# Kernel tuning notes

Hardware: AMD Instinct MI355X
Metric: run time of the kernel (lower is better)

The kernel has to match this reference:

```python
import jax, jax.numpy as jnp
import numpy as np

DIM = 512; H = 8; DH = 64; M = 256; ITERS = 6; K = 33  # residual conv kernel


def _pinv(x, iters=ITERS):
    # Moore-Penrose iterative pseudo-inverse (lucidrains moore_penrose_iter_pinv)
    abs_x = jnp.abs(x)
    denom = abs_x.sum(-1).max() * abs_x.sum(-2).max()  # global max of col/row sums
    z = jnp.swapaxes(x, -1, -2) / denom
    I = jnp.eye(x.shape[-1], dtype=x.dtype)
    for _ in range(iters):
        xz = x @ z
        z = 0.25 * z @ (13. * I - xz @ (15. * I - xz @ (7. * I - xz)))
    return z


def setup_inputs() -> dict:
    key = jax.random.key(0)
    ks = jax.random.split(key, 5)
    b, n = 4, 4096
    inner = H * DH
    x = jax.random.normal(ks[0], (b, n, DIM), jnp.float32)
    ln_g = jnp.ones((DIM,), jnp.float32)
    ln_b = jnp.zeros((DIM,), jnp.float32)
    w_qkv = jax.random.normal(ks[1], (DIM, 3 * inner), jnp.float32) / np.sqrt(DIM).astype(np.float32)
    w_out = jax.random.normal(ks[2], (inner, DIM), jnp.float32) / np.sqrt(inner).astype(np.float32)
    b_out = jnp.zeros((DIM,), jnp.float32)
    res_w = jax.random.normal(ks[3], (H, K), jnp.float32) * 0.02  # depthwise conv weight per head
    return {"x": x, "ln_g": ln_g, "ln_b": ln_b, "w_qkv": w_qkv,
            "w_out": w_out, "b_out": b_out, "res_w": res_w}


def reference(x, ln_g, ln_b, w_qkv, w_out, b_out, res_w):
    b, n, d = x.shape
    # LayerNorm (eps=1e-5, biased variance, like torch)
    mu = x.mean(-1, keepdims=True)
    var = ((x - mu) ** 2).mean(-1, keepdims=True)
    xn = (x - mu) * jax.lax.rsqrt(var + 1e-5) * ln_g + ln_b
    # QKV projection, no bias
    qkv = xn @ w_qkv  # [b, n, 3*h*dh]
    q, k, v = jnp.split(qkv, 3, axis=-1)
    tohd = lambda t: t.reshape(b, n, H, DH).transpose(0, 2, 1, 3)  # b h n d
    q = tohd(q) * (DH ** -0.5)
    k = tohd(k)
    v = tohd(v)
    # landmarks: mean over consecutive blocks of l = n // M (n divisible by M here)
    l = n // M
    q_l = q.reshape(b, H, M, l, DH).mean(3)  # b h m d
    k_l = k.reshape(b, H, M, l, DH).mean(3)
    attn1 = jax.nn.softmax(jnp.einsum('bhid,bhjd->bhij', q, k_l), axis=-1)   # b h n m
    attn2 = jax.nn.softmax(jnp.einsum('bhid,bhjd->bhij', q_l, k_l), axis=-1)  # b h m m
    attn3 = jax.nn.softmax(jnp.einsum('bhid,bhjd->bhij', q_l, k), axis=-1)   # b h m n
    out = (attn1 @ _pinv(attn2)) @ (attn3 @ v)  # b h n dh
    # depthwise residual conv over sequence dim (Conv2d(heads, heads, (33,1), groups=heads))
    res = jax.lax.conv_general_dilated(
        v, res_w.reshape(H, 1, K, 1), (1, 1), ((K // 2, K // 2), (0, 0)),
        feature_group_count=H, dimension_numbers=('NCHW', 'OIHW', 'NCHW'))
    out = out + res
    # merge heads + output projection (dropout is identity at eval)
    out = out.transpose(0, 2, 1, 3).reshape(b, n, H * DH) @ w_out + b_out
    # TransLayer residual
    return x + out
```

## Files before the change

### kernel.cpp

```cpp
#include <hip/hip_runtime.h>
#include <hip/hip_bf16.h>

#define SEQ    4096
#define NBAT   4
#define NHEAD  8
#define NBH    32
#define DMODEL 512
#define DHEAD  64
#define NLM    256

typedef __attribute__((ext_vector_type(8))) short s8v;
typedef __attribute__((ext_vector_type(4))) float f4v;

__device__ __forceinline__ float b2f(unsigned short u){
  union { unsigned int i; float f; } v; v.i = ((unsigned int)u) << 16; return v.f;
}
__device__ __forceinline__ unsigned short f2b(float f){
  union { float f; unsigned int i; } v; v.f = f;
  unsigned int r = v.i + 0x7fffu + ((v.i >> 16) & 1u);
  return (unsigned short)(r >> 16);
}
__device__ __forceinline__ s8v ldg8(const unsigned short* p){
  return *reinterpret_cast<const s8v*>(p);
}
__device__ __forceinline__ f4v mfma16(s8v a, s8v b, f4v c){
  return __builtin_amdgcn_mfma_f32_16x16x32_bf16(a, b, c, 0, 0, 0);
}
__device__ __forceinline__ f4v zero4(){ f4v z; z[0]=0.f; z[1]=0.f; z[2]=0.f; z[3]=0.f; return z; }

__global__ void k_prep(const float* __restrict__ wqkv, const float* __restrict__ wout,
                       unsigned short* __restrict__ wqkvT, unsigned short* __restrict__ woutT,
                       unsigned int* __restrict__ denomU, float* __restrict__ w2f){
  int t = blockIdx.x*256 + threadIdx.x;
  if (t == 0) denomU[0] = 0u;
  if (t < 786432){ int kk = t/1536, n = t%1536; wqkvT[(size_t)n*512 + kk] = f2b(wqkv[t]); }
  else { int t2 = t - 786432; if (t2 < 262144){ int kk = t2/512, n = t2%512; woutT[(size_t)n*512 + kk] = f2b(wout[t2]); } }
  if (t < 524288) w2f[t] = 0.f;
}

__global__ __launch_bounds__(256) void k_ln(const float* __restrict__ x, const float* __restrict__ g,
                                            const float* __restrict__ be, unsigned short* __restrict__ xn){
  int row = blockIdx.x*4 + (threadIdx.x>>6);
  int l = threadIdx.x & 63;
  const float* xr = x + (size_t)row*DMODEL;
  float4 a = *(const float4*)(xr + l*4);
  float4 b = *(const float4*)(xr + 256 + l*4);
  float s = a.x+a.y+a.z+a.w + b.x+b.y+b.z+b.w;
  float q = a.x*a.x+a.y*a.y+a.z*a.z+a.w*a.w + b.x*b.x+b.y*b.y+b.z*b.z+b.w*b.w;
  #pragma unroll
  for (int m=1;m<64;m<<=1){ s += __shfl_xor(s,m); q += __shfl_xor(q,m); }
  float mean = s*(1.f/DMODEL);
  float rstd = rsqrtf(q*(1.f/DMODEL) - mean*mean + 1e-5f);
  int c0 = l*4, c1 = 256 + l*4;
  float av[4] = {a.x,a.y,a.z,a.w}, bv[4] = {b.x,b.y,b.z,b.w};
  ushort4 u0, u1;
  unsigned short* p0 = (unsigned short*)&u0; unsigned short* p1 = (unsigned short*)&u1;
  #pragma unroll
  for (int e=0;e<4;++e){
    p0[e] = f2b((av[e]-mean)*rstd*g[c0+e] + be[c0+e]);
    p1[e] = f2b((bv[e]-mean)*rstd*g[c1+e] + be[c1+e]);
  }
  *(ushort4*)(xn + (size_t)row*DMODEL + c0) = u0;
  *(ushort4*)(xn + (size_t)row*DMODEL + c1) = u1;
}

__device__ __forceinline__ void gemm512(const unsigned short* __restrict__ A, const unsigned short* __restrict__ B,
                                        int m0, int n0, int t, unsigned short* lA, unsigned short* lB,
                                        f4v acc[4][4]){
  int w = t>>6, l = t&63;
  int wm = (w&1)*64, wn = (w>>1)*64;
  for (int ks=0; ks<16; ++ks){
    #pragma unroll
    for (int it=0; it<2; ++it){
      int cid = it*256 + t; int r = cid>>2, kof = (cid&3)<<3;
      *(s8v*)&lA[r*40 + kof] = ldg8(&A[(size_t)(m0+r)*DMODEL + ks*32 + kof]);
      *(s8v*)&lB[r*40 + kof] = ldg8(&B[(size_t)(n0+r)*DMODEL + ks*32 + kof]);
    }
    __syncthreads();
    s8v af[4], bf[4];
    #pragma unroll
    for (int i=0;i<4;++i) af[i] = *(s8v*)&lA[(wm+i*16+(l&15))*40 + ((l>>4)<<3)];
    #pragma unroll
    for (int j=0;j<4;++j) bf[j] = *(s8v*)&lB[(wn+j*16+(l&15))*40 + ((l>>4)<<3)];
    #pragma unroll
    for (int i=0;i<4;++i)
      #pragma unroll
      for (int j=0;j<4;++j) acc[i][j] = mfma16(af[i], bf[j], acc[i][j]);
    __syncthreads();
  }
}

__global__ __launch_bounds__(256) void k_gqkv(const unsigned short* __restrict__ xn, const unsigned short* __restrict__ wT,
                                              unsigned short* __restrict__ q, unsigned short* __restrict__ k,
                                              unsigned short* __restrict__ v, unsigned short* __restrict__ vT){
  __shared__ unsigned short lA[128*40], lB[128*40];
  int bid = blockIdx.x; int mblk = bid/12, nblk = bid%12;
  int m0 = mblk*128, n0 = nblk*128;
  int t = threadIdx.x;
  f4v acc[4][4];
  #pragma unroll
  for (int i=0;i<4;++i)
    #pragma unroll
    for (int j=0;j<4;++j) acc[i][j] = zero4();
  gemm512(xn, wT, m0, n0, t, lA, lB, acc);
  int w = t>>6, l = t&63; int wm = (w&1)*64, wn = (w>>1)*64;
  int part = nblk >> 2;
  int coff = (nblk & 3) * 128;
  unsigned short* dst = (part==0) ? q : (part==1) ? k : v;
  float scale = (part==0) ? 0.125f : 1.f;
  #pragma unroll
  for (int i=0;i<4;++i)
  #pragma unroll
  for (int j=0;j<4;++j){
    int colg = coff + wn + j*16 + (l&15);
    int h = colg>>6, c = colg&63;
    #pragma unroll
    for (int r=0;r<4;++r){
      int rowg = m0 + wm + i*16 + ((l>>4)<<2) + r;
      int b = rowg>>12, n = rowg&4095;
      unsigned short val = f2b(acc[i][j][r]*scale);
      dst[ (((size_t)(b*NHEAD + h))*SEQ + n)*DHEAD + c ] = val;
      if (part == 2)
        vT[ (((size_t)(b*NHEAD + h))*DHEAD + c)*SEQ + n ] = val;
    }
  }
}

__global__ __launch_bounds__(256) void k_gout(const unsigned short* __restrict__ ao, const unsigned short* __restrict__ wT,
                                              const float* __restrict__ x, const float* __restrict__ bo,
                                              float* __restrict__ out){
  __shared__ unsigned short lA[128*40], lB[128*40];
  int bid = blockIdx.x; int mblk = bid>>2, nblk = bid&3;
  int m0 = mblk*128, n0 = nblk*128;
  int t = threadIdx.x;
  f4v acc[4][4];
  #pragma unroll
  for (int i=0;i<4;++i)
    #pragma unroll
    for (int j=0;j<4;++j) acc[i][j] = zero4();
  gemm512(ao, wT, m0, n0, t, lA, lB, acc);
  int w = t>>6, l = t&63; int wm = (w&1)*64, wn = (w>>1)*64;
  #pragma unroll
  for (int i=0;i<4;++i)
  #pragma unroll
  for (int j=0;j<4;++j){
    int colg = n0 + wn + j*16 + (l&15);
    #pragma unroll
    for (int r=0;r<4;++r){
      int rowg = m0 + wm + i*16 + ((l>>4)<<2) + r;
      size_t ad = (size_t)rowg*DMODEL + colg;
      out[ad] = acc[i][j][r] + x[ad] + bo[colg];
    }
  }
}

__global__ void k_lmk(const unsigned short* __restrict__ q, const unsigned short* __restrict__ k,
                      unsigned short* __restrict__ ql, unsigned short* __restrict__ kl){
  int tg = blockIdx.x*256 + threadIdx.x;
  int c4 = (tg&15)*4, m = (tg>>4)&255, bh = tg>>12;
  const unsigned short* qb = q + ((size_t)bh*SEQ + m*16)*DHEAD + c4;
  const unsigned short* kb = k + ((size_t)bh*SEQ + m*16)*DHEAD + c4;
  float s0=0.f,s1=0.f,s2=0.f,s3=0.f, t0=0.f,t1=0.f,t2=0.f,t3=0.f;
  #pragma unroll
  for (int j=0;j<16;++j){
    ushort4 uq = *(const ushort4*)(qb + (size_t)j*DHEAD);
    ushort4 uk = *(const ushort4*)(kb + (size_t)j*DHEAD);
    s0+=b2f(uq.x); s1+=b2f(uq.y); s2+=b2f(uq.z); s3+=b2f(uq.w);
    t0+=b2f(uk.x); t1+=b2f(uk.y); t2+=b2f(uk.z); t3+=b2f(uk.w);
  }
  ushort4 oq, ok;
  oq.x=f2b(s0*(1.f/16.f)); oq.y=f2b(s1*(1.f/16.f)); oq.z=f2b(s2*(1.f/16.f)); oq.w=f2b(s3*(1.f/16.f));
  ok.x=f2b(t0*(1.f/16.f)); ok.y=f2b(t1*(1.f/16.f)); ok.z=f2b(t2*(1.f/16.f)); ok.w=f2b(t3*(1.f/16.f));
  *(ushort4*)(ql + ((size_t)bh*NLM + m)*DHEAD + c4) = oq;
  *(ushort4*)(kl + ((size_t)bh*NLM + m)*DHEAD + c4) = ok;
}

__global__ __launch_bounds__(512) void k_attn2(const unsigned short* __restrict__ ql, const unsigned short* __restrict__ kl,
                                               unsigned short* __restrict__ a2, unsigned short* __restrict__ a2t,
                                               unsigned int* __restrict__ denomU){
  __shared__ float cs[256];
  int bh = blockIdx.x; int t = threadIdx.x; int w = t>>6, l = t&63;
  const unsigned short* Q = ql + (size_t)bh*NLM*DHEAD;
  const unsigned short* K = kl + (size_t)bh*NLM*DHEAD;
  f4v acc[2][16];
  #pragma unroll
  for (int i=0;i<2;++i)
    #pragma unroll
    for (int j=0;j<16;++j) acc[i][j] = zero4();
  int m0 = w*32;
  #pragma unroll
  for (int ks=0; ks<2; ++ks){
    int kk = ks*32 + ((l>>4)<<3);
    s8v af0 = ldg8(&Q[(size_t)(m0 + (l&15))*DHEAD + kk]);
    s8v af1 = ldg8(&Q[(size_t)(m0 + 16 + (l&15))*DHEAD + kk]);
    #pragma unroll
    for (int j=0;j<16;++j){
      s8v bf = ldg8(&K[(size_t)(j*16 + (l&15))*DHEAD + kk]);
      acc[0][j] = mfma16(af0, bf, acc[0][j]);
      acc[1][j] = mfma16(af1, bf, acc[1][j]);
    }
  }
  #pragma unroll
  for (int i=0;i<2;++i)
  #pragma unroll
  for (int r=0;r<4;++r){
    float mx = -1e30f;
    #pragma unroll
    for (int j=0;j<16;++j) mx = fmaxf(mx, acc[i][j][r]);
    #pragma unroll
    for (int mm=1;mm<16;mm<<=1) mx = fmaxf(mx, __shfl_xor(mx,mm));
    float sm = 0.f;
    #pragma unroll
    for (int j=0;j<16;++j){ float p = __expf(acc[i][j][r]-mx); acc[i][j][r]=p; sm += p; }
    #pragma unroll
    for (int mm=1;mm<16;mm<<=1) sm += __shfl_xor(sm,mm);
    float inv = 1.f/sm;
    #pragma unroll
    for (int j=0;j<16;++j) acc[i][j][r] *= inv;
  }
  for (int e=t; e<256; e+=512) cs[e] = 0.f;
  __syncthreads();
  size_t b0 = (size_t)bh*NLM*NLM;
  #pragma unroll
  for (int i=0;i<2;++i)
  #pragma unroll
  for (int j=0;j<16;++j){
    int col = j*16 + (l&15);
    int rowb = m0 + i*16 + ((l>>4)<<2);
    float csp = 0.f;
    #pragma unroll
    for (int r=0;r<4;++r){
      float p = acc[i][j][r];
      unsigned short pb = f2b(p);
      a2 [b0 + (size_t)(rowb+r)*NLM + col] = pb;
      a2t[b0 + (size_t)col*NLM + rowb + r] = pb;
      csp += p;
    }
    csp += __shfl_xor(csp, 16); csp += __shfl_xor(csp, 32);
    if ((l>>4) == 0) atomicAdd(&cs[col], csp);
  }
  __syncthreads();
  if (t < 256) atomicMax(denomU, __float_as_uint(cs[t]));
}

__global__ __launch_bounds__(512) void k_attn3p(const unsigned short* __restrict__ ql, const unsigned short* __restrict__ kk_,
                                                unsigned short* __restrict__ p3, int bhoff){
  __shared__ float redm[16][8], reds[16][8];
  int bh = bhoff + (blockIdx.x>>4); int m0 = (blockIdx.x&15)*16;
  int t = threadIdx.x, w = t>>6, l = t&63;
  const unsigned short* Q  = ql  + (size_t)bh*NLM*DHEAD;
  const unsigned short* Kp = kk_ + (size_t)bh*SEQ*DHEAD;
  f4v acc[32];
  #pragma unroll
  for (int j=0;j<32;++j) acc[j] = zero4();
  #pragma unroll
  for (int ks=0; ks<2; ++ks){
    int kof = ks*32 + ((l>>4)<<3);
    s8v af = ldg8(&Q[(size_t)(m0 + (l&15))*DHEAD + kof]);
    #pragma unroll
    for (int j=0;j<32;++j){
      int n = w*512 + j*16 + (l&15);
      s8v bf = ldg8(&Kp[(size_t)n*DHEAD + kof]);
      acc[j] = mfma16(af, bf, acc[j]);
    }
  }
  int g = l>>4;
  #pragma unroll
  for (int r=0;r<4;++r){
    int rl = g*4 + r;
    float mx = -1e30f;
    #pragma unroll
    for (int j=0;j<32;++j) mx = fmaxf(mx, acc[j][r]);
    #pragma unroll
    for (int mm=1;mm<16;mm<<=1) mx = fmaxf(mx, __shfl_xor(mx,mm));
    if ((l&15)==0) redm[rl][w] = mx;
  }
  __syncthreads();
  #pragma unroll
  for (int r=0;r<4;++r){
    int rl = g*4 + r;
    float mx = redm[rl][0];
    #pragma unroll
    for (int ww=1;ww<8;++ww) mx = fmaxf(mx, redm[rl][ww]);
    float sm = 0.f;
    #pragma unroll
    for (int j=0;j<32;++j){ float p = __expf(acc[j][r]-mx); acc[j][r]=p; sm += p; }
    #pragma unroll
    for (int mm=1;mm<16;mm<<=1) sm += __shfl_xor(sm,mm);
    if ((l&15)==0) reds[rl][w] = sm;
  }
  __syncthreads();
  size_t pb = ((size_t)(bh-bhoff)*NLM + m0)*SEQ;
  #pragma unroll
  for (int r=0;r<4;++r){
    int rl = g*4 + r;
    float sm = 0.f;
    #pragma unroll
    for (int ww=0;ww<8;++ww) sm += reds[rl][ww];
    float inv = 1.f/sm;
    #pragma unroll
    for (int j=0;j<32;++j)
      p3[pb + (size_t)rl*SEQ + w*512 + j*16 + (l&15)] = f2b(acc[j][r]*inv);
  }
}

__global__ __launch_bounds__(256) void k_w2(const unsigned short* __restrict__ p3, const unsigned short* __restrict__ vt,
                                            float* __restrict__ w2f, int bhoff){
  int bid = blockIdx.x;
  int kspl = bid & 7, mblk = (bid>>3)&1, bhl = bid>>4;
  int t = threadIdx.x, w = t>>6, l = t&63;
  int m0 = mblk*128 + w*32;
  const unsigned short* P  = p3 + (size_t)bhl*NLM*SEQ;
  const unsigned short* VT = vt + (size_t)(bhoff+bhl)*DHEAD*SEQ;
  f4v acc[2][4];
  #pragma unroll
  for (int i=0;i<2;++i)
    #pragma unroll
    for (int j=0;j<4;++j) acc[i][j] = zero4();
  for (int ks = kspl*16; ks < kspl*16+16; ++ks){
    int kof = ks*32 + ((l>>4)<<3);
    s8v af0 = ldg8(&P[(size_t)(m0 + (l&15))*SEQ + kof]);
    s8v af1 = ldg8(&P[(size_t)(m0 + 16 + (l&15))*SEQ + kof]);
    #pragma unroll
    for (int j=0;j<4;++j){
      s8v bf = ldg8(&VT[(size_t)(j*16 + (l&15))*SEQ + kof]);
      acc[0][j] = mfma16(af0, bf, acc[0][j]);
      acc[1][j] = mfma16(af1, bf, acc[1][j]);
    }
  }
  float* W = w2f + (size_t)(bhoff+bhl)*NLM*DHEAD;
  #pragma unroll
  for (int i=0;i<2;++i)
  #pragma unroll
  for (int j=0;j<4;++j)
    #pragma unroll
    for (int r=0;r<4;++r)
      atomicAdd(&W[(size_t)(m0 + i*16 + ((l>>4)<<2) + r)*DHEAD + j*16 + (l&15)], acc[i][j][r]);
}

__global__ void k_w2t(const float* __restrict__ w2f, unsigned short* __restrict__ w2t){
  int tg = blockIdx.x*256 + threadIdx.x;
  int m = tg&255, c = (tg>>8)&63, bh = tg>>14;
  w2t[((size_t)bh*DHEAD + c)*NLM + m] = f2b(w2f[((size_t)bh*NLM + m)*DHEAD + c]);
}

__global__ __launch_bounds__(256) void k_conv(const unsigned short* __restrict__ v, const float* __restrict__ rw,
                                              unsigned short* __restrict__ cf){
  int bh = blockIdx.x >> 6;
  int n0 = (blockIdx.x & 63) * 64;
  int h = bh & 7, b = bh >> 3;
  int t = threadIdx.x;
  int tx = t & 15, ty = t >> 4;
  int c4 = tx * 4;
  int nb = n0 + ty * 4;
  const unsigned short* vb = v + ((size_t)bh * SEQ) * DHEAD + c4;
  ushort4 val[36];
  #pragma unroll
  for (int i = 0; i < 36; ++i){
    int nn = nb - 16 + i;
    if (nn >= 0 && nn < SEQ) val[i] = *(const ushort4*)(vb + (size_t)nn * DHEAD);
    else { val[i].x = 0; val[i].y = 0; val[i].z = 0; val[i].w = 0; }
  }
  float wgt[33];
  #pragma unroll
  for (int o = 0; o < 33; ++o) wgt[o] = rw[h*33 + o];
  #pragma unroll
  for (int i = 0; i < 4; ++i){
    float s0 = 0.f, s1 = 0.f, s2 = 0.f, s3 = 0.f;
    #pragma unroll
    for (int o = 0; o < 33; ++o){
      ushort4 u = val[i + o];
      float w0 = wgt[o];
      s0 += w0 * b2f(u.x); s1 += w0 * b2f(u.y);
      s2 += w0 * b2f(u.z); s3 += w0 * b2f(u.w);
    }
    ushort4 ov;
    ov.x = f2b(s0); ov.y = f2b(s1); ov.z = f2b(s2); ov.w = f2b(s3);
    size_t ad = ((size_t)b * SEQ + (nb + i)) * DMODEL + h * DHEAD + c4;
    *(ushort4*)(cf + ad) = ov;
  }
}

__device__ __forceinline__ void pcore(const unsigned short* __restrict__ Ab, const unsigned short* __restrict__ Bb,
                                      int m0, int n0, int l, f4v acc[4][4]){
  for (int ks=0; ks<8; ++ks){
    int kk = ks*32 + ((l>>4)<<3);
    s8v af[4], bf[4];
    #pragma unroll
    for (int i=0;i<4;++i) af[i] = ldg8(&Ab[(size_t)(m0 + i*16 + (l&15))*256 + kk]);
    #pragma unroll
    for (int j=0;j<4;++j) bf[j] = ldg8(&Bb[(size_t)(n0 + j*16 + (l&15))*256 + kk]);
    #pragma unroll
    for (int i=0;i<4;++i)
      #pragma unroll
      for (int j=0;j<4;++j) acc[i][j] = mfma16(af[i], bf[j], acc[i][j]);
  }
}

__global__ __launch_bounds__(64) void k_pg1(const unsigned short* __restrict__ A, const unsigned short* __restrict__ BT,
                                            unsigned short* __restrict__ oN, unsigned short* __restrict__ oT,
                                            int sdiv, const unsigned int* __restrict__ denomU){
  int bid = blockIdx.x;
  int bh = bid>>4, tt = bid&15;
  int m0 = (tt>>2)*64, n0 = (tt&3)*64;
  int l = threadIdx.x;
  const unsigned short* Ab = A + (size_t)bh*65536;
  const unsigned short* Bb = BT + (size_t)bh*65536;
  f4v acc[4][4];
  #pragma unroll
  for (int i=0;i<4;++i)
    #pragma unroll
    for (int j=0;j<4;++j) acc[i][j] = zero4();
  pcore(Ab, Bb, m0, n0, l, acc);
  float s = sdiv ? 1.f/__uint_as_float(denomU[0]) : 1.f;
  #pragma unroll
  for (int i=0;i<4;++i)
  #pragma unroll
  for (int j=0;j<4;++j){
    int col = n0 + j*16 + (l&15);
    #pragma unroll
    for (int r=0;r<4;++r){
      int row = m0 + i*16 + ((l>>4)<<2) + r;
      unsigned short ob = f2b(acc[i][j][r]*s);
      oN[(size_t)bh*65536 + (size_t)row*256 + col] = ob;
      oT[(size_t)bh*65536 + (size_t)col*256 + row] = ob;
    }
  }
}

__global__ __launch_bounds__(64) void k_pg2(const unsigned short* __restrict__ xzN, const unsigned short* __restrict__ xzT,
                                            const unsigned short* __restrict__ zsrc,
                                            unsigned short* __restrict__ CT, unsigned short* __restrict__ PN,
                                            int sdiv, const unsigned int* __restrict__ denomU){
  int bid = blockIdx.x;
  int part = bid>>9; bid &= 511;
  int bh = bid>>4, tt = bid&15;
  int m0 = (tt>>2)*64, n0 = (tt&3)*64;
  int l = threadIdx.x;
  const unsigned short* Ab = (part==0 ? xzN : zsrc) + (size_t)bh*65536;
  const unsigned short* Bb = xzT + (size_t)bh*65536;
  f4v acc[4][4];
  #pragma unroll
  for (int i=0;i<4;++i)
    #pragma unroll
    for (int j=0;j<4;++j) acc[i][j] = zero4();
  pcore(Ab, Bb, m0, n0, l, acc);
  if (part == 0){
    #pragma unroll
    for (int i=0;i<4;++i)
    #pragma unroll
    for (int j=0;j<4;++j){
      int col = n0 + j*16 + (l&15);
      #pragma unroll
      for (int r=0;r<4;++r){
        int row = m0 + i*16 + ((l>>4)<<2) + r;
        float xv = b2f(xzN[(size_t)bh*65536 + (size_t)row*256 + col]);
        CT[(size_t)bh*65536 + (size_t)col*256 + row] = f2b(7.f*xv - acc[i][j][r]);
      }
    }
  } else {
    float s = sdiv ? 1.f/__uint_as_float(denomU[0]) : 1.f;
    #pragma unroll
    for (int i=0;i<4;++i)
    #pragma unroll
    for (int j=0;j<4;++j){
      int col = n0 + j*16 + (l&15);
      #pragma unroll
      for (int r=0;r<4;++r){
        int row = m0 + i*16 + ((l>>4)<<2) + r;
        PN[(size_t)bh*65536 + (size_t)row*256 + col] = f2b(acc[i][j][r]*s);
      }
    }
  }
}

__global__ __launch_bounds__(64) void k_pg3(const unsigned short* __restrict__ PN, const unsigned short* __restrict__ CT,
                                            const unsigned short* __restrict__ zsrc,
                                            unsigned short* __restrict__ zN, unsigned short* __restrict__ zT,
                                            int sdiv, const unsigned int* __restrict__ denomU){
  int bid = blockIdx.x;
  int bh = bid>>4, tt = bid&15;
  int m0 = (tt>>2)*64, n0 = (tt&3)*64;
  int l = threadIdx.x;
  const unsigned short* Ab = PN + (size_t)bh*65536;
  const unsigned short* Bb = CT + (size_t)bh*65536;
  f4v acc[4][4];
  #pragma unroll
  for (int i=0;i<4;++i)
    #pragma unroll
    for (int j=0;j<4;++j) acc[i][j] = zero4();
  pcore(Ab, Bb, m0, n0, l, acc);
  float zs = sdiv ? 1.f/__uint_as_float(denomU[0]) : 1.f;
  #pragma unroll
  for (int i=0;i<4;++i)
  #pragma unroll
  for (int j=0;j<4;++j){
    int col = n0 + j*16 + (l&15);
    #pragma unroll
    for (int r=0;r<4;++r){
      int row = m0 + i*16 + ((l>>4)<<2) + r;
      float zv = b2f(zsrc[(size_t)bh*65536 + (size_t)row*256 + col])*zs;
      float pv = b2f(PN  [(size_t)bh*65536 + (size_t)row*256 + col]);
      float res = 0.25f*(13.f*zv - 15.f*pv + acc[i][j][r]);
      unsigned short ob = f2b(res);
      zN[(size_t)bh*65536 + (size_t)row*256 + col] = ob;
      zT[(size_t)bh*65536 + (size_t)col*256 + row] = ob;
    }
  }
}

template<bool WN, bool WT>
__global__ __launch_bounds__(64) void k_pgemm(
    const unsigned short* __restrict__ A, const unsigned short* __restrict__ BT,
    unsigned short* __restrict__ oN, unsigned short* __restrict__ oT,
    int mt, int nt, long strA, long strBT, long strON, long strOT)
{
  int bid = blockIdx.x;
  int nper = mt*nt;
  int bh = bid/nper, tt = bid%nper;
  int m0 = (tt/nt)*64, n0 = (tt%nt)*64;
  const unsigned short* Ab = A + (size_t)bh*strA;
  const unsigned short* Bb = BT + (size_t)bh*strBT;
  int l = threadIdx.x;
  f4v acc[4][4];
  #pragma unroll
  for (int i=0;i<4;++i)
    #pragma unroll
    for (int j=0;j<4;++j) acc[i][j] = zero4();
  pcore(Ab, Bb, m0, n0, l, acc);
  #pragma unroll
  for (int i=0;i<4;++i)
  #pragma unroll
  for (int j=0;j<4;++j){
    int col = n0 + j*16 + (l&15);
    #pragma unroll
    for (int r=0;r<4;++r){
      int row = m0 + i*16 + ((l>>4)<<2) + r;
      unsigned short ob = f2b(acc[i][j][r]);
      if constexpr (WN) oN[(size_t)bh*strON + (size_t)row*256 + col] = ob;
      if constexpr (WT) oT[(size_t)bh*strOT + (size_t)col*256 + row] = ob;
    }
  }
}

__global__ __launch_bounds__(256) void k_attn1(const unsigned short* __restrict__ qb, const unsigned short* __restrict__ kl,
                                               const unsigned short* __restrict__ ut, const unsigned short* __restrict__ cf,
                                               unsigned short* __restrict__ ao){
  int bh = blockIdx.x>>6;
  int t = threadIdx.x, w = t>>6, l = t&63;
  int q0 = ((blockIdx.x&63)<<6) + (w<<4);
  int g = l>>4, qi = l&15;
  const unsigned short* Q = qb + (size_t)bh*SEQ*DHEAD;
  const unsigned short* K = kl + (size_t)bh*NLM*DHEAD;
  f4v acc[16];
  #pragma unroll
  for (int j=0;j<16;++j) acc[j] = zero4();
  #pragma unroll
  for (int ks=0;ks<2;++ks){
    int kk = ks*32 + g*8;
    s8v bq = ldg8(&Q[(size_t)(q0+qi)*DHEAD + kk]);
    #pragma unroll
    for (int j=0;j<16;++j){
      s8v ak = ldg8(&K[(size_t)(j*16+qi)*DHEAD + kk]);
      acc[j] = mfma16(ak, bq, acc[j]);
    }
  }
  float mx = -1e30f;
  #pragma unroll
  for (int j=0;j<16;++j)
    mx = fmaxf(mx, fmaxf(fmaxf(acc[j][0],acc[j][1]), fmaxf(acc[j][2],acc[j][3])));
  mx = fmaxf(mx, __shfl_xor(mx,16));
  mx = fmaxf(mx, __shfl_xor(mx,32));
  float sm = 0.f;
  #pragma unroll
  for (int j=0;j<16;++j)
    #pragma unroll
    for (int r=0;r<4;++r){ float p = __expf(acc[j][r]-mx); acc[j][r]=p; sm += p; }
  sm += __shfl_xor(sm,16); sm += __shfl_xor(sm,32);
  float inv = 1.f/sm;
  unsigned int pku[32];
  #pragma unroll
  for (int j=0;j<16;++j){
    pku[2*j+0] = (unsigned int)f2b(acc[j][0]*inv) | ((unsigned int)f2b(acc[j][1]*inv)<<16);
    pku[2*j+1] = (unsigned int)f2b(acc[j][2]*inv) | ((unsigned int)f2b(acc[j][3]*inv)<<16);
  }
  const unsigned short* U = ut + (size_t)bh*DHEAD*NLM;
  f4v oacc[4];
  #pragma unroll
  for (int j=0;j<4;++j) oacc[j] = zero4();
  int sl0 = ((g&1)*2)*16 + qi;
  int jsel = g>>1;
  #pragma unroll
  for (int ks=0;ks<8;++ks){
    unsigned int w0a = (unsigned int)__shfl((int)pku[4*ks+0], sl0, 64);
    unsigned int w1a = (unsigned int)__shfl((int)pku[4*ks+1], sl0, 64);
    unsigned int w0b = (unsigned int)__shfl((int)pku[4*ks+2], sl0, 64);
    unsigned int w1b = (unsigned int)__shfl((int)pku[4*ks+3], sl0, 64);
    unsigned int w2a = (unsigned int)__shfl((int)pku[4*ks+0], sl0+16, 64);
    unsigned int w3a = (unsigned int)__shfl((int)pku[4*ks+1], sl0+16, 64);
    unsigned int w2b = (unsigned int)__shfl((int)pku[4*ks+2], sl0+16, 64);
    unsigned int w3b = (unsigned int)__shfl((int)pku[4*ks+3], sl0+16, 64);
    unsigned int wv0 = jsel ? w0b : w0a;
    unsigned int wv1 = jsel ? w1b : w1a;
    unsigned int wv2 = jsel ? w2b : w2a;
    unsigned int wv3 = jsel ? w3b : w3a;
    s8v af;
    af[0] = (short)(wv0&0xffff); af[1] = (short)(wv0>>16);
    af[2] = (short)(wv1&0xffff); af[3] = (short)(wv1>>16);
    af[4] = (short)(wv2&0xffff); af[5] = (short)(wv2>>16);
    af[6] = (short)(wv3&0xffff); af[7] = (short)(wv3>>16);
    int mk = ks*32 + g*8;
    #pragma unroll
    for (int j=0;j<4;++j){
      s8v bu = ldg8(&U[(size_t)(j*16+qi)*NLM + mk]);
      oacc[j] = mfma16(af, bu, oacc[j]);
    }
  }
  int b = bh>>3, h = bh&7;
  #pragma unroll
  for (int j=0;j<4;++j){
    int c = j*16 + qi;
    #pragma unroll
    for (int r=0;r<4;++r){
      int n = q0 + g*4 + r;
      size_t ad = ((size_t)(b*SEQ + n))*DMODEL + h*DHEAD + c;
      ao[ad] = f2b(oacc[j][r] + b2f(cf[ad]));
    }
  }
}

extern "C" void kernel_launch(void* const* d_in, const int* in_sizes, int n_in,
                              void* d_out, int out_size, void* d_ws, size_t ws_size,
                              hipStream_t stream){
  const float* x    = (const float*)d_in[0];
  const float* lng  = (const float*)d_in[1];
  const float* lnb  = (const float*)d_in[2];
  const float* wqkv = (const float*)d_in[3];
  const float* wout = (const float*)d_in[4];
  const float* bout = (const float*)d_in[5];
  const float* resw = (const float*)d_in[6];
  float* out = (float*)d_out;

  char* ws = (char*)d_ws;
  size_t off = 0;
  auto alloc = [&](size_t bytes)->char*{ char* p = ws + off; off += (bytes + 255) & ~(size_t)255; return p; };

  unsigned short* wqkvT = (unsigned short*)alloc((size_t)1536*512*2);
  unsigned short* woutT = (unsigned short*)alloc((size_t)512*512*2);
  unsigned int*   denomU= (unsigned int*)  alloc(256);
  unsigned short* xn    = (unsigned short*)alloc((size_t)16384*512*2);
  unsigned short* zA  = xn;
  unsigned short* zAT = xn + (size_t)1*NBH*NLM*NLM;
  unsigned short* zB  = xn + (size_t)2*NBH*NLM*NLM;
  unsigned short* zBT = xn + (size_t)3*NBH*NLM*NLM;
  unsigned short* q   = (unsigned short*)alloc((size_t)NBH*SEQ*DHEAD*2);
  unsigned short* kb  = (unsigned short*)alloc((size_t)NBH*SEQ*DHEAD*2);
  unsigned short* ao  = kb;
  unsigned short* v   = (unsigned short*)alloc((size_t)NBH*SEQ*DHEAD*2);
  unsigned short* vT  = (unsigned short*)alloc((size_t)NBH*DHEAD*SEQ*2);
  unsigned short* ql  = (unsigned short*)alloc((size_t)NBH*NLM*DHEAD*2);
  unsigned short* kl  = (unsigned short*)alloc((size_t)NBH*NLM*DHEAD*2);
  unsigned short* a2  = (unsigned short*)alloc((size_t)NBH*NLM*NLM*2);
  unsigned short* a2t = (unsigned short*)alloc((size_t)NBH*NLM*NLM*2);
  char* R1            = alloc((size_t)16*NLM*SEQ*2);
  unsigned short* p3  = (unsigned short*)R1;
  unsigned short* convf = (unsigned short*)R1;
  unsigned short* xz  = (unsigned short*)alloc((size_t)NBH*NLM*NLM*2);
  unsigned short* xzt = (unsigned short*)alloc((size_t)NBH*NLM*NLM*2);
  unsigned short* pn  = (unsigned short*)alloc((size_t)NBH*NLM*NLM*2);
  unsigned short* ctb = (unsigned short*)alloc((size_t)NBH*NLM*NLM*2);
  float*          w2f = (float*)         alloc((size_t)NBH*NLM*DHEAD*4);
  unsigned short* w2t = (unsigned short*)alloc((size_t)NBH*DHEAD*NLM*2);
  unsigned short* ut  = (unsigned short*)alloc((size_t)NBH*DHEAD*NLM*2);
  (void)ws_size; (void)in_sizes; (void)n_in; (void)out_size;

  k_prep<<<4096,256,0,stream>>>(wqkv, wout, wqkvT, woutT, denomU, w2f);
  k_ln  <<<4096,256,0,stream>>>(x, lng, lnb, xn);
  k_gqkv<<<1536,256,0,stream>>>(xn, wqkvT, q, kb, v, vT);
  k_lmk <<<512,256,0,stream>>>(q, kb, ql, kl);
  k_attn2<<<32,512,0,stream>>>(ql, kl, a2, a2t, denomU);
  for (int half=0; half<2; ++half){
    k_attn3p<<<256,512,0,stream>>>(ql, kb, p3, half*16);
    k_w2    <<<256,256,0,stream>>>(p3, vT, w2f, half*16);
  }
  k_w2t <<<2048,256,0,stream>>>(w2f, w2t);
  k_conv<<<2048,256,0,stream>>>(v, resw, convf);

  unsigned short* zN_[2] = {zA, zB};
  unsigned short* zT_[2] = {zAT, zBT};
  for (int it = 0; it < 6; ++it){
    const unsigned short* BT   = (it==0) ? a2  : zT_[(it-1)&1];
    const unsigned short* zsrc = (it==0) ? a2t : zN_[(it-1)&1];
    int sdiv = (it==0) ? 1 : 0;
    k_pg1<<<512 ,64,0,stream>>>(a2, BT, xz, xzt, sdiv, denomU);
    k_pg2<<<1024,64,0,stream>>>(xz, xzt, zsrc, ctb, pn, sdiv, denomU);
    k_pg3<<<512 ,64,0,stream>>>(pn, ctb, zsrc, zN_[it&1], zT_[it&1], sdiv, denomU);
  }
  k_pgemm<false,true><<<128,64,0,stream>>>(zN_[1], w2t, (unsigned short*)nullptr, ut, 4,1, 65536L,16384L,0L,16384L);

  k_attn1<<<2048,256,0,stream>>>(q, kl, ut, convf, ao);
  k_gout <<<512,256,0,stream>>>(ao, woutT, x, bout, out);
}
```

Baseline: 546.3 us.

## Fuse attn3 softmax and V product into flash-style kernel; use direct-to-LDS GEMM loads

```diff
diff --git a/kernel.cpp b/kernel.cpp
--- a/kernel.cpp
+++ b/kernel.cpp
@@ -27,15 +27,18 @@
   return __builtin_amdgcn_mfma_f32_16x16x32_bf16(a, b, c, 0, 0, 0);
 }
 __device__ __forceinline__ f4v zero4(){ f4v z; z[0]=0.f; z[1]=0.f; z[2]=0.f; z[3]=0.f; return z; }
+__device__ __forceinline__ void gload16(const unsigned short* g, unsigned short* l){
+  __builtin_amdgcn_global_load_lds((const __attribute__((address_space(1))) unsigned int*)g,
+                                   (__attribute__((address_space(3))) unsigned int*)l, 16, 0, 0);
+}
 
 __global__ void k_prep(const float* __restrict__ wqkv, const float* __restrict__ wout,
                        unsigned short* __restrict__ wqkvT, unsigned short* __restrict__ woutT,
-                       unsigned int* __restrict__ denomU, float* __restrict__ w2f){
+                       unsigned int* __restrict__ denomU){
   int t = blockIdx.x*256 + threadIdx.x;
   if (t == 0) denomU[0] = 0u;
   if (t < 786432){ int kk = t/1536, n = t%1536; wqkvT[(size_t)n*512 + kk] = f2b(wqkv[t]); }
   else { int t2 = t - 786432; if (t2 < 262144){ int kk = t2/512, n = t2%512; woutT[(size_t)n*512 + kk] = f2b(wout[t2]); } }
-  if (t < 524288) w2f[t] = 0.f;
 }
 
 __global__ __launch_bounds__(256) void k_ln(const float* __restrict__ x, const float* __restrict__ g,
@@ -64,24 +67,43 @@
   *(ushort4*)(xn + (size_t)row*DMODEL + c1) = u1;
 }
 
-__device__ __forceinline__ void gemm512(const unsigned short* __restrict__ A, const unsigned short* __restrict__ B,
-                                        int m0, int n0, int t, unsigned short* lA, unsigned short* lB,
-                                        f4v acc[4][4]){
+__device__ __forceinline__ void gemm512v2(const unsigned short* __restrict__ A, const unsigned short* __restrict__ B,
+                                          int m0, int n0, int t, unsigned short* lA, unsigned short* lB,
+                                          f4v acc[4][4]){
   int w = t>>6, l = t&63;
   int wm = (w&1)*64, wn = (w>>1)*64;
+  int g = l>>4, qi = l&15;
+  int rs = (w<<4) + (l>>2);
+  int s0 = l&3;
+  int c0 = ((s0 ^ ((rs>>1)&3)) << 3);
+  int r1 = rs + 64;
+  int c1 = ((s0 ^ ((r1>>1)&3)) << 3);
+  const unsigned short* gA0 = A + (size_t)(m0+rs)*DMODEL + c0;
+  const unsigned short* gA1 = A + (size_t)(m0+r1)*DMODEL + c1;
+  const unsigned short* gB0 = B + (size_t)(n0+rs)*DMODEL + c0;
+  const unsigned short* gB1 = B + (size_t)(n0+r1)*DMODEL + c1;
+  unsigned short* dA0 = lA + (w<<9);
+  unsigned short* dA1 = lA + 2048 + (w<<9);
+  unsigned short* dB0 = lB + (w<<9);
+  unsigned short* dB1 = lB + 2048 + (w<<9);
+  int aofs[4], bofs[4];
+  #pragma unroll
+  for (int i=0;i<4;++i){
+    int ra = wm + i*16 + qi;
+    aofs[i] = ra*32 + ((g ^ ((ra>>1)&3))<<3);
+    int rb = wn + i*16 + qi;
+    bofs[i] = rb*32 + ((g ^ ((rb>>1)&3))<<3);
+  }
   for (int ks=0; ks<16; ++ks){
-    #pragma unroll
-    for (int it=0; it<2; ++it){
-      int cid = it*256 + t; int r = cid>>2, kof = (cid&3)<<3;
-      *(s8v*)&lA[r*40 + kof] = ldg8(&A[(size_t)(m0+r)*DMODEL + ks*32 + kof]);
-      *(s8v*)&lB[r*40 + kof] = ldg8(&B[(size_t)(n0+r)*DMODEL + ks*32 + kof]);
-    }
+    gload16(gA0, dA0); gload16(gA1, dA1);
+    gload16(gB0, dB0); gload16(gB1, dB1);
+    gA0 += 32; gA1 += 32; gB0 += 32; gB1 += 32;
     __syncthreads();
     s8v af[4], bf[4];
     #pragma unroll
-    for (int i=0;i<4;++i) af[i] = *(s8v*)&lA[(wm+i*16+(l&15))*40 + ((l>>4)<<3)];
-    #pragma unroll
-    for (int j=0;j<4;++j) bf[j] = *(s8v*)&lB[(wn+j*16+(l&15))*40 + ((l>>4)<<3)];
+    for (int i=0;i<4;++i) af[i] = *(s8v*)&lA[aofs[i]];
+    #pragma unroll
+    for (int j=0;j<4;++j) bf[j] = *(s8v*)&lB[bofs[j]];
     #pragma unroll
     for (int i=0;i<4;++i)
       #pragma unroll
@@ -93,7 +115,7 @@
 __global__ __launch_bounds__(256) void k_gqkv(const unsigned short* __restrict__ xn, const unsigned short* __restrict__ wT,
                                               unsigned short* __restrict__ q, unsigned short* __restrict__ k,
                                               unsigned short* __restrict__ v, unsigned short* __restrict__ vT){
-  __shared__ unsigned short lA[128*40], lB[128*40];
+  __shared__ __align__(16) unsigned short lA[4096], lB[4096];
   int bid = blockIdx.x; int mblk = bid/12, nblk = bid%12;
   int m0 = mblk*128, n0 = nblk*128;
   int t = threadIdx.x;
@@ -102,7 +124,7 @@
   for (int i=0;i<4;++i)
     #pragma unroll
     for (int j=0;j<4;++j) acc[i][j] = zero4();
-  gemm512(xn, wT, m0, n0, t, lA, lB, acc);
+  gemm512v2(xn, wT, m0, n0, t, lA, lB, acc);
   int w = t>>6, l = t&63; int wm = (w&1)*64, wn = (w>>1)*64;
   int part = nblk >> 2;
   int coff = (nblk & 3) * 128;
@@ -129,7 +151,7 @@
 __global__ __launch_bounds__(256) void k_gout(const unsigned short* __restrict__ ao, const unsigned short* __restrict__ wT,
                                               const float* __restrict__ x, const float* __restrict__ bo,
                                               float* __restrict__ out){
-  __shared__ unsigned short lA[128*40], lB[128*40];
+  __shared__ __align__(16) unsigned short lA[4096], lB[4096];
   int bid = blockIdx.x; int mblk = bid>>2, nblk = bid&3;
   int m0 = mblk*128, n0 = nblk*128;
   int t = threadIdx.x;
@@ -138,7 +160,7 @@
   for (int i=0;i<4;++i)
     #pragma unroll
     for (int j=0;j<4;++j) acc[i][j] = zero4();
-  gemm512(ao, wT, m0, n0, t, lA, lB, acc);
+  gemm512v2(ao, wT, m0, n0, t, lA, lB, acc);
   int w = t>>6, l = t&63; int wm = (w&1)*64, wn = (w>>1)*64;
   #pragma unroll
   for (int i=0;i<4;++i)
@@ -243,105 +265,101 @@
   if (t < 256) atomicMax(denomU, __float_as_uint(cs[t]));
 }
 
-__global__ __launch_bounds__(512) void k_attn3p(const unsigned short* __restrict__ ql, const unsigned short* __restrict__ kk_,
-                                                unsigned short* __restrict__ p3, int bhoff){
-  __shared__ float redm[16][8], reds[16][8];
-  int bh = bhoff + (blockIdx.x>>4); int m0 = (blockIdx.x&15)*16;
+__global__ __launch_bounds__(128) void k_a3w2(const unsigned short* __restrict__ ql, const unsigned short* __restrict__ kb,
+                                              const unsigned short* __restrict__ vT, unsigned short* __restrict__ w2t){
+  int bh = blockIdx.x >> 3;
   int t = threadIdx.x, w = t>>6, l = t&63;
-  const unsigned short* Q  = ql  + (size_t)bh*NLM*DHEAD;
-  const unsigned short* Kp = kk_ + (size_t)bh*SEQ*DHEAD;
-  f4v acc[32];
-  #pragma unroll
-  for (int j=0;j<32;++j) acc[j] = zero4();
-  #pragma unroll
-  for (int ks=0; ks<2; ++ks){
-    int kof = ks*32 + ((l>>4)<<3);
-    s8v af = ldg8(&Q[(size_t)(m0 + (l&15))*DHEAD + kof]);
-    #pragma unroll
-    for (int j=0;j<32;++j){
-      int n = w*512 + j*16 + (l&15);
-      s8v bf = ldg8(&Kp[(size_t)n*DHEAD + kof]);
-      acc[j] = mfma16(af, bf, acc[j]);
-    }
-  }
-  int g = l>>4;
-  #pragma unroll
-  for (int r=0;r<4;++r){
-    int rl = g*4 + r;
-    float mx = -1e30f;
-    #pragma unroll
-    for (int j=0;j<32;++j) mx = fmaxf(mx, acc[j][r]);
-    #pragma unroll
-    for (int mm=1;mm<16;mm<<=1) mx = fmaxf(mx, __shfl_xor(mx,mm));
-    if ((l&15)==0) redm[rl][w] = mx;
-  }
-  __syncthreads();
-  #pragma unroll
-  for (int r=0;r<4;++r){
-    int rl = g*4 + r;
-    float mx = redm[rl][0];
-    #pragma unroll
-    for (int ww=1;ww<8;++ww) mx = fmaxf(mx, redm[rl][ww]);
-    float sm = 0.f;
-    #pragma unroll
-    for (int j=0;j<32;++j){ float p = __expf(acc[j][r]-mx); acc[j][r]=p; sm += p; }
-    #pragma unroll
-    for (int mm=1;mm<16;mm<<=1) sm += __shfl_xor(sm,mm);
-    if ((l&15)==0) reds[rl][w] = sm;
-  }
-  __syncthreads();
-  size_t pb = ((size_t)(bh-bhoff)*NLM + m0)*SEQ;
-  #pragma unroll
-  for (int r=0;r<4;++r){
-    int rl = g*4 + r;
-    float sm = 0.f;
-    #pragma unroll
-    for (int ww=0;ww<8;++ww) sm += reds[rl][ww];
-    float inv = 1.f/sm;
-    #pragma unroll
-    for (int j=0;j<32;++j)
-      p3[pb + (size_t)rl*SEQ + w*512 + j*16 + (l&15)] = f2b(acc[j][r]*inv);
-  }
-}
-
-__global__ __launch_bounds__(256) void k_w2(const unsigned short* __restrict__ p3, const unsigned short* __restrict__ vt,
-                                            float* __restrict__ w2f, int bhoff){
-  int bid = blockIdx.x;
-  int kspl = bid & 7, mblk = (bid>>3)&1, bhl = bid>>4;
-  int t = threadIdx.x, w = t>>6, l = t&63;
-  int m0 = mblk*128 + w*32;
-  const unsigned short* P  = p3 + (size_t)bhl*NLM*SEQ;
-  const unsigned short* VT = vt + (size_t)(bhoff+bhl)*DHEAD*SEQ;
-  f4v acc[2][4];
-  #pragma unroll
-  for (int i=0;i<2;++i)
-    #pragma unroll
-    for (int j=0;j<4;++j) acc[i][j] = zero4();
-  for (int ks = kspl*16; ks < kspl*16+16; ++ks){
-    int kof = ks*32 + ((l>>4)<<3);
-    s8v af0 = ldg8(&P[(size_t)(m0 + (l&15))*SEQ + kof]);
-    s8v af1 = ldg8(&P[(size_t)(m0 + 16 + (l&15))*SEQ + kof]);
+  int q0 = ((blockIdx.x & 7) << 5) + (w<<4);
+  int g = l>>4, qi = l&15;
+  const unsigned short* Q = ql + ((size_t)bh*NLM + q0)*DHEAD;
+  const unsigned short* K = kb + (size_t)bh*SEQ*DHEAD;
+  const unsigned short* V = vT + (size_t)bh*DHEAD*SEQ;
+  float m_run = -1e30f, den = 0.f;
+  f4v oacc[4];
+  #pragma unroll
+  for (int j=0;j<4;++j) oacc[j] = zero4();
+  int sl0 = ((g&1)*2)*16 + qi;
+  int jsel = g>>1;
+  for (int kc=0; kc<16; ++kc){
+    const unsigned short* Kc = K + (size_t)kc*256*DHEAD;
+    f4v acc[16];
+    #pragma unroll
+    for (int j=0;j<16;++j) acc[j] = zero4();
+    #pragma unroll
+    for (int ks=0;ks<2;++ks){
+      int kk = ks*32 + g*8;
+      s8v bq = ldg8(&Q[(size_t)qi*DHEAD + kk]);
+      #pragma unroll
+      for (int j=0;j<16;++j){
+        s8v ak = ldg8(&Kc[(size_t)(j*16+qi)*DHEAD + kk]);
+        acc[j] = mfma16(ak, bq, acc[j]);
+      }
+    }
+    float cm = -1e30f;
+    #pragma unroll
+    for (int j=0;j<16;++j)
+      cm = fmaxf(cm, fmaxf(fmaxf(acc[j][0],acc[j][1]), fmaxf(acc[j][2],acc[j][3])));
+    cm = fmaxf(cm, __shfl_xor(cm,16));
+    cm = fmaxf(cm, __shfl_xor(cm,32));
+    float nm = fmaxf(m_run, cm);
+    float f = __expf(m_run - nm);
+    m_run = nm;
+    float ls = 0.f;
+    unsigned int pku[32];
+    #pragma unroll
+    for (int j=0;j<16;++j){
+      float p0 = __expf(acc[j][0]-nm), p1 = __expf(acc[j][1]-nm);
+      float p2 = __expf(acc[j][2]-nm), p3 = __expf(acc[j][3]-nm);
+      ls += (p0+p1)+(p2+p3);
+      pku[2*j+0] = (unsigned int)f2b(p0) | ((unsigned int)f2b(p1)<<16);
+      pku[2*j+1] = (unsigned int)f2b(p2) | ((unsigned int)f2b(p3)<<16);
+    }
+    den = den*f + ls;
+    float fr0 = __shfl(f, g*4+0, 64), fr1 = __shfl(f, g*4+1, 64);
+    float fr2 = __shfl(f, g*4+2, 64), fr3 = __shfl(f, g*4+3, 64);
     #pragma unroll
     for (int j=0;j<4;++j){
-      s8v bf = ldg8(&VT[(size_t)(j*16 + (l&15))*SEQ + kof]);
-      acc[0][j] = mfma16(af0, bf, acc[0][j]);
-      acc[1][j] = mfma16(af1, bf, acc[1][j]);
-    }
-  }
-  float* W = w2f + (size_t)(bhoff+bhl)*NLM*DHEAD;
-  #pragma unroll
-  for (int i=0;i<2;++i)
-  #pragma unroll
-  for (int j=0;j<4;++j)
-    #pragma unroll
-    for (int r=0;r<4;++r)
-      atomicAdd(&W[(size_t)(m0 + i*16 + ((l>>4)<<2) + r)*DHEAD + j*16 + (l&15)], acc[i][j][r]);
-}
-
-__global__ void k_w2t(const float* __restrict__ w2f, unsigned short* __restrict__ w2t){
-  int tg = blockIdx.x*256 + threadIdx.x;
-  int m = tg&255, c = (tg>>8)&63, bh = tg>>14;
-  w2t[((size_t)bh*DHEAD + c)*NLM + m] = f2b(w2f[((size_t)bh*NLM + m)*DHEAD + c]);
+      oacc[j][0]*=fr0; oacc[j][1]*=fr1; oacc[j][2]*=fr2; oacc[j][3]*=fr3;
+    }
+    #pragma unroll
+    for (int ks=0;ks<8;++ks){
+      unsigned int w0a = (unsigned int)__shfl((int)pku[4*ks+0], sl0, 64);
+      unsigned int w1a = (unsigned int)__shfl((int)pku[4*ks+1], sl0, 64);
+      unsigned int w0b = (unsigned int)__shfl((int)pku[4*ks+2], sl0, 64);
+      unsigned int w1b = (unsigned int)__shfl((int)pku[4*ks+3], sl0, 64);
+      unsigned int w2a = (unsigned int)__shfl((int)pku[4*ks+0], sl0+16, 64);
+      unsigned int w3a = (unsigned int)__shfl((int)pku[4*ks+1], sl0+16, 64);
+      unsigned int w2b = (unsigned int)__shfl((int)pku[4*ks+2], sl0+16, 64);
+      unsigned int w3b = (unsigned int)__shfl((int)pku[4*ks+3], sl0+16, 64);
+      unsigned int wv0 = jsel ? w0b : w0a;
+      unsigned int wv1 = jsel ? w1b : w1a;
+      unsigned int wv2 = jsel ? w2b : w2a;
+      unsigned int wv3 = jsel ? w3b : w3a;
+      s8v af;
+      af[0] = (short)(wv0&0xffff); af[1] = (short)(wv0>>16);
+      af[2] = (short)(wv1&0xffff); af[3] = (short)(wv1>>16);
+      af[4] = (short)(wv2&0xffff); af[5] = (short)(wv2>>16);
+      af[6] = (short)(wv3&0xffff); af[7] = (short)(wv3>>16);
+      int mk = ks*32 + g*8;
+      #pragma unroll
+      for (int j=0;j<4;++j){
+        s8v bu = ldg8(&V[(size_t)(j*16+qi)*SEQ + kc*256 + mk]);
+        oacc[j] = mfma16(af, bu, oacc[j]);
+      }
+    }
+  }
+  den += __shfl_xor(den,16); den += __shfl_xor(den,32);
+  float inv = 1.f/den;
+  float ir0 = __shfl(inv, g*4+0, 64), ir1 = __shfl(inv, g*4+1, 64);
+  float ir2 = __shfl(inv, g*4+2, 64), ir3 = __shfl(inv, g*4+3, 64);
+  #pragma unroll
+  for (int j=0;j<4;++j){
+    size_t cb = ((size_t)bh*DHEAD + j*16 + qi)*NLM + q0 + g*4;
+    w2t[cb+0] = f2b(oacc[j][0]*ir0);
+    w2t[cb+1] = f2b(oacc[j][1]*ir1);
+    w2t[cb+2] = f2b(oacc[j][2]*ir2);
+    w2t[cb+3] = f2b(oacc[j][3]*ir3);
+  }
 }
 
 __global__ __launch_bounds__(256) void k_conv(const unsigned short* __restrict__ v, const float* __restrict__ rw,
@@ -662,28 +680,21 @@
   unsigned short* kl  = (unsigned short*)alloc((size_t)NBH*NLM*DHEAD*2);
   unsigned short* a2  = (unsigned short*)alloc((size_t)NBH*NLM*NLM*2);
   unsigned short* a2t = (unsigned short*)alloc((size_t)NBH*NLM*NLM*2);
-  char* R1            = alloc((size_t)16*NLM*SEQ*2);
-  unsigned short* p3  = (unsigned short*)R1;
-  unsigned short* convf = (unsigned short*)R1;
+  unsigned short* convf = (unsigned short*)alloc((size_t)NBAT*SEQ*DMODEL*2);
   unsigned short* xz  = (unsigned short*)alloc((size_t)NBH*NLM*NLM*2);
   unsigned short* xzt = (unsigned short*)alloc((size_t)NBH*NLM*NLM*2);
   unsigned short* pn  = (unsigned short*)alloc((size_t)NBH*NLM*NLM*2);
   unsigned short* ctb = (unsigned short*)alloc((size_t)NBH*NLM*NLM*2);
-  float*          w2f = (float*)         alloc((size_t)NBH*NLM*DHEAD*4);
   unsigned short* w2t = (unsigned short*)alloc((size_t)NBH*DHEAD*NLM*2);
   unsigned short* ut  = (unsigned short*)alloc((size_t)NBH*DHEAD*NLM*2);
   (void)ws_size; (void)in_sizes; (void)n_in; (void)out_size;
 
-  k_prep<<<4096,256,0,stream>>>(wqkv, wout, wqkvT, woutT, denomU, w2f);
+  k_prep<<<4096,256,0,stream>>>(wqkv, wout, wqkvT, woutT, denomU);
   k_ln  <<<4096,256,0,stream>>>(x, lng, lnb, xn);
   k_gqkv<<<1536,256,0,stream>>>(xn, wqkvT, q, kb, v, vT);
   k_lmk <<<512,256,0,stream>>>(q, kb, ql, kl);
   k_attn2<<<32,512,0,stream>>>(ql, kl, a2, a2t, denomU);
-  for (int half=0; half<2; ++half){
-    k_attn3p<<<256,512,0,stream>>>(ql, kb, p3, half*16);
-    k_w2    <<<256,256,0,stream>>>(p3, vT, w2f, half*16);
-  }
-  k_w2t <<<2048,256,0,stream>>>(w2f, w2t);
+  k_a3w2<<<256,128,0,stream>>>(ql, kb, vT, w2t);
   k_conv<<<2048,256,0,stream>>>(v, resw, convf);
 
   unsigned short* zN_[2] = {zA, zB};
```

New measurement: 559.6 us. 2.4% more time.
